# Kernel optimization log

Hardware: AMD Instinct MI355X
Metric: run time of the kernel (lower is better)

Reference implementation:

```python
import jax, jax.numpy as jnp
import numpy as np

B, T, C = 8, 1024, 768
H = 12
HS = C // H  # 64


def setup_inputs() -> dict:
    key = jax.random.key(0)
    ks = jax.random.split(key, 6)
    s = C ** -0.5
    x = jax.random.normal(ks[0], (B, T, C), dtype=jnp.float32)
    Wq = jax.random.normal(ks[1], (H, C, HS), dtype=jnp.float32) * s
    Wk = jax.random.normal(ks[2], (H, C, HS), dtype=jnp.float32) * s
    Wv = jax.random.normal(ks[3], (H, C, HS), dtype=jnp.float32) * s
    Wproj = jax.random.normal(ks[4], (C, C), dtype=jnp.float32) * s
    bproj = jax.random.normal(ks[5], (C,), dtype=jnp.float32) * 0.01
    return {"x": x, "Wq": Wq, "Wk": Wk, "Wv": Wv, "Wproj": Wproj, "bproj": bproj}


def reference(x, Wq, Wk, Wv, Wproj, bproj):
    # per-head projections (equivalent to stacked per-head nn.Linear, bias=False)
    q = jnp.einsum('btc,hcd->bhtd', x, Wq)
    k = jnp.einsum('btc,hcd->bhtd', x, Wk)
    v = jnp.einsum('btc,hcd->bhtd', x, Wv)
    scale = HS ** -0.5
    scores = jnp.einsum('bhtd,bhsd->bhts', q, k) * scale  # [B,H,T,T]
    causal = jnp.tril(jnp.ones((T, T), dtype=bool))
    scores = jnp.where(causal, scores, -jnp.inf)
    weights = jax.nn.softmax(scores, axis=-1)
    out = jnp.einsum('bhts,bhsd->bhtd', weights, v)  # [B,H,T,HS]
    out = out.transpose(0, 2, 1, 3).reshape(B, T, C)  # concat heads
    # output projection (dropout is identity in eval mode)
    return out @ Wproj.T + bproj
```

## Files before the change

kernel.cpp:

```cpp
#include <hip/hip_runtime.h>


typedef short bf16x8 __attribute__((ext_vector_type(8)));
typedef float f32x4 __attribute__((ext_vector_type(4)));

static __device__ __forceinline__ unsigned short f2bf(float f) {
  unsigned int u = __float_as_uint(f);
  u += 0x7fffu + ((u >> 16) & 1u);
  return (unsigned short)(u >> 16);
}

static __device__ __forceinline__ void gl_lds16(const void* g, void* l) {
  __builtin_amdgcn_global_load_lds(
      (const __attribute__((address_space(1))) unsigned int*)g,
      (__attribute__((address_space(3))) unsigned int*)l, 16, 0, 0);
}

__global__ __launch_bounds__(256) void k_prep(
    const float* __restrict__ x, const float* __restrict__ Wproj,
    const float* __restrict__ Wq, const float* __restrict__ Wk,
    const float* __restrict__ Wv,
    unsigned short* __restrict__ xb, unsigned short* __restrict__ wp,
    unsigned short* __restrict__ wt) {
  __shared__ float tb[64][65];
  const int bx = blockIdx.x;
  const int tid = threadIdx.x;
  if (bx < 6720) {
    const float* src = (bx < 6144) ? x : Wproj;
    unsigned short* dst = (bx < 6144) ? xb : wp;
    int i = (bx < 6144 ? bx : bx - 6144) * 256 + tid;
    float4 f = ((const float4*)src)[i];
    ushort4 o;
    o.x = f2bf(f.x); o.y = f2bf(f.y); o.z = f2bf(f.z); o.w = f2bf(f.w);
    ((ushort4*)dst)[i] = o;
    return;
  }
  const int idx = bx - 6720;
  const int c0 = (idx % 12) * 64;
  const int hq = idx / 12;
  const int qi = hq / 12, h = hq % 12;
  const float* W = (qi == 0) ? Wq : ((qi == 1) ? Wk : Wv);
  {
    int rowb = tid >> 4;
    int col4 = (tid & 15) * 4;
#pragma unroll
    for (int it = 0; it < 4; ++it) {
      int c = it * 16 + rowb;
      float4 f = *(const float4*)(W + (h * 768 + c0 + c) * 64 + col4);
      tb[c][col4] = f.x; tb[c][col4 + 1] = f.y; tb[c][col4 + 2] = f.z; tb[c][col4 + 3] = f.w;
    }
  }
  __syncthreads();
#pragma unroll
  for (int it = 0; it < 2; ++it) {
    int slot = it * 256 + tid;
    int d = slot >> 3, cg = (slot & 7) * 8;
    union { unsigned short a[8]; uint4 v; } o;
#pragma unroll
    for (int j = 0; j < 8; ++j) o.a[j] = f2bf(tb[cg + j][d]);
    *(uint4*)(wt + (qi * 768 + h * 64 + d) * 768 + c0 + cg) = o.v;
  }
}

__global__ __launch_bounds__(256) void k_gemm_qk(
    const unsigned short* __restrict__ xb,
    const unsigned short* __restrict__ wt,
    unsigned short* __restrict__ qkv) {
  __shared__ unsigned short As[128 * 32];
  __shared__ unsigned short Bs[128 * 32];
  const int tid = threadIdx.x;
  const int w = tid >> 6, lane = tid & 63, quad = lane >> 4, lr = lane & 15;
  const int wm = w >> 1, wn = w & 1;
  const int m0 = blockIdx.x * 128, n0 = blockIdx.y * 128;

  f32x4 acc[4][4] = {};

  const int srow = w * 16 + (lane >> 2);
  const int scol = (lane & 3) * 8;
  const unsigned short* ga0 = xb + (m0 + srow) * 768 + scol;
  const unsigned short* ga1 = ga0 + 64 * 768;
  const unsigned short* gb0 = wt + (n0 + srow) * 768 + scol;
  const unsigned short* gb1 = gb0 + 64 * 768;
  unsigned short* la0 = &As[(w * 16) * 32];
  unsigned short* la1 = la0 + 64 * 32;
  unsigned short* lb0 = &Bs[(w * 16) * 32];
  unsigned short* lb1 = lb0 + 64 * 32;

  for (int k0 = 0; k0 < 768; k0 += 32) {
    gl_lds16(ga0 + k0, la0);
    gl_lds16(ga1 + k0, la1);
    gl_lds16(gb0 + k0, lb0);
    gl_lds16(gb1 + k0, lb1);
    __syncthreads();
    bf16x8 af[4], bfr[4];
#pragma unroll
    for (int i = 0; i < 4; ++i)
      af[i] = *(const bf16x8*)(&As[(wm * 64 + i * 16 + lr) * 32 + quad * 8]);
#pragma unroll
    for (int j = 0; j < 4; ++j)
      bfr[j] = *(const bf16x8*)(&Bs[(wn * 64 + j * 16 + lr) * 32 + quad * 8]);
#pragma unroll
    for (int i = 0; i < 4; ++i)
#pragma unroll
      for (int j = 0; j < 4; ++j)
        acc[i][j] = __builtin_amdgcn_mfma_f32_16x16x32_bf16(af[i], bfr[j], acc[i][j], 0, 0, 0);
    __syncthreads();
  }

  const int b = m0 >> 10, t0 = m0 & 1023;
#pragma unroll
  for (int j = 0; j < 4; ++j) {
    int n = n0 + wn * 64 + j * 16 + lr;
    int qi = n >> 9 >> 1;
    qi = n / 768;
    int rr = n - qi * 768;
    int h = rr >> 6, d = rr & 63;
#pragma unroll
    for (int i = 0; i < 4; ++i) {
#pragma unroll
      for (int r = 0; r < 4; ++r) {
        int t = t0 + wm * 64 + i * 16 + quad * 4 + r;
        qkv[(size_t)(((qi * 8 + b) * 12 + h) * 1024 + t) * 64 + d] = f2bf(acc[i][j][r]);
      }
    }
  }
}

__global__ __launch_bounds__(256) void k_gemm_v(
    const unsigned short* __restrict__ xb,
    const unsigned short* __restrict__ wt,
    unsigned short* __restrict__ vt) {
  __shared__ unsigned short As[128 * 32];
  __shared__ unsigned short Bs[128 * 32];
  const int tid = threadIdx.x;
  const int w = tid >> 6, lane = tid & 63, quad = lane >> 4, lr = lane & 15;
  const int wm = w >> 1, wn = w & 1;
  const int m0 = blockIdx.x * 128, n0 = blockIdx.y * 128;

  f32x4 acc[4][4] = {};

  const int srow = w * 16 + (lane >> 2);
  const int scol = (lane & 3) * 8;
  const unsigned short* ga0 = xb + (m0 + srow) * 768 + scol;
  const unsigned short* ga1 = ga0 + 64 * 768;
  const unsigned short* gb0 = wt + (size_t)(1536 + n0 + srow) * 768 + scol;
  const unsigned short* gb1 = gb0 + 64 * 768;
  unsigned short* la0 = &As[(w * 16) * 32];
  unsigned short* la1 = la0 + 64 * 32;
  unsigned short* lb0 = &Bs[(w * 16) * 32];
  unsigned short* lb1 = lb0 + 64 * 32;

  for (int k0 = 0; k0 < 768; k0 += 32) {
    gl_lds16(ga0 + k0, la0);
    gl_lds16(ga1 + k0, la1);
    gl_lds16(gb0 + k0, lb0);
    gl_lds16(gb1 + k0, lb1);
    __syncthreads();
    bf16x8 af[4], bfr[4];
#pragma unroll
    for (int i = 0; i < 4; ++i)
      af[i] = *(const bf16x8*)(&As[(wm * 64 + i * 16 + lr) * 32 + quad * 8]);
#pragma unroll
    for (int j = 0; j < 4; ++j)
      bfr[j] = *(const bf16x8*)(&Bs[(wn * 64 + j * 16 + lr) * 32 + quad * 8]);
#pragma unroll
    for (int i = 0; i < 4; ++i)
#pragma unroll
      for (int j = 0; j < 4; ++j)
        acc[i][j] = __builtin_amdgcn_mfma_f32_16x16x32_bf16(af[i], bfr[j], acc[i][j], 0, 0, 0);
    __syncthreads();
  }

  const int b = m0 >> 10, t0 = m0 & 1023;
#pragma unroll
  for (int j = 0; j < 4; ++j) {
    int rr = n0 + wn * 64 + j * 16 + lr;
    int h = rr >> 6, d = rr & 63;
    unsigned short* vrow = vt + (size_t)((b * 12 + h) * 64 + d) * 1024;
#pragma unroll
    for (int i = 0; i < 4; ++i) {
      int t = t0 + wm * 64 + i * 16 + quad * 4;
      union { unsigned short a[4]; uint2 u; } o;
#pragma unroll
      for (int r = 0; r < 4; ++r) o.a[r] = f2bf(acc[i][j][r]);
      *(uint2*)(vrow + t) = o.u;
    }
  }
}

__global__ __launch_bounds__(256) void k_attn(
    const unsigned short* __restrict__ qkv,
    const unsigned short* __restrict__ Vtg,
    unsigned short* __restrict__ attn) {
  __shared__ unsigned short Kbuf[2][64 * 64];
  __shared__ unsigned short Vbuf[2][64 * 64];
  __shared__ unsigned short Pbuf[4][32 * 68];
  const int tid = threadIdx.x;
  const int w = tid >> 6, lane = tid & 63, quad = lane >> 4, lr = lane & 15;
  const int hb = blockIdx.x;
  const int qb = 7 - (int)blockIdx.y;
  const int h = hb % 12, b = hb / 12;
  const int HT = 65536;
  const unsigned short* Q  = qkv + (b * 12 + h) * HT;
  const unsigned short* K  = qkv + (96 + b * 12 + h) * HT;
  const unsigned short* Vt = Vtg + (b * 12 + h) * HT;

  bf16x8 aq[2][2];
#pragma unroll
  for (int i = 0; i < 2; ++i)
#pragma unroll
    for (int hf = 0; hf < 2; ++hf)
      aq[i][hf] = *(const bf16x8*)(Q + (qb * 128 + w * 32 + i * 16 + lr) * 64 + hf * 32 + quad * 8);

  f32x4 accO[2][4] = {};
  float lsum[2][4] = {};

  const int nc = 2 * qb + 2;
  const float c1 = 0.125f * 1.4426950408889634f;
  const float c0 = -4.0f * 1.4426950408889634f;

  auto stage = [&](int bi, int sc) {
#pragma unroll
    for (int j = 0; j < 2; ++j) {
      int row = w * 16 + j * 8 + (lane >> 3);
      int c8 = (lane & 7) ^ (row & 7);
      gl_lds16(K + (sc * 64 + row) * 64 + c8 * 8, &Kbuf[bi][(w * 16 + j * 8) * 64]);
      gl_lds16(Vt + row * 1024 + sc * 64 + c8 * 8, &Vbuf[bi][(w * 16 + j * 8) * 64]);
    }
  };

  stage(0, 0);
  for (int sc = 0; sc < nc; ++sc) {
    __syncthreads();
    if (sc + 1 < nc) stage((sc + 1) & 1, sc + 1);
    const unsigned short* Kl = Kbuf[sc & 1];
    const unsigned short* Vl = Vbuf[sc & 1];

    f32x4 accS[2][4];
#pragma unroll
    for (int i = 0; i < 2; ++i)
#pragma unroll
      for (int nt = 0; nt < 4; ++nt) {
        f32x4 z = {};
#pragma unroll
        for (int hf = 0; hf < 2; ++hf) {
          int s = nt * 16 + lr;
          bf16x8 kb = *(const bf16x8*)(Kl + (s * 8 + ((4 * hf + quad) ^ (s & 7))) * 8);
          z = __builtin_amdgcn_mfma_f32_16x16x32_bf16(aq[i][hf], kb, z, 0, 0, 0);
        }
        accS[i][nt] = z;
      }

#pragma unroll
    for (int i = 0; i < 2; ++i) {
      const int base_i = qb * 128 + w * 32 + i * 16;
      const bool needmask = (sc * 64 + 63 > base_i);
#pragma unroll
      for (int r = 0; r < 4; ++r) {
        int tg = base_i + quad * 4 + r;
#pragma unroll
        for (int nt = 0; nt < 4; ++nt) {
          float p = __builtin_amdgcn_exp2f(fmaf(accS[i][nt][r], c1, c0));
          if (needmask && (sc * 64 + nt * 16 + lr > tg)) p = 0.f;
          lsum[i][r] += p;
          Pbuf[w][(i * 16 + quad * 4 + r) * 68 + nt * 16 + lr] = f2bf(p);
        }
      }
    }

#pragma unroll
    for (int i = 0; i < 2; ++i) {
      bf16x8 pa[2];
#pragma unroll
      for (int hf = 0; hf < 2; ++hf)
        pa[hf] = *(const bf16x8*)(&Pbuf[w][(i * 16 + lr) * 68 + hf * 32 + quad * 8]);
#pragma unroll
      for (int ntd = 0; ntd < 4; ++ntd) {
        int d = ntd * 16 + lr;
#pragma unroll
        for (int hf = 0; hf < 2; ++hf) {
          bf16x8 vb = *(const bf16x8*)(Vl + (d * 8 + ((4 * hf + quad) ^ (d & 7))) * 8);
          accO[i][ntd] = __builtin_amdgcn_mfma_f32_16x16x32_bf16(pa[hf], vb, accO[i][ntd], 0, 0, 0);
        }
      }
    }
  }

  float linv[2][4];
#pragma unroll
  for (int i = 0; i < 2; ++i)
#pragma unroll
    for (int r = 0; r < 4; ++r) {
      float l = lsum[i][r];
      l += __shfl_xor(l, 1);
      l += __shfl_xor(l, 2);
      l += __shfl_xor(l, 4);
      l += __shfl_xor(l, 8);
      linv[i][r] = 1.0f / l;
    }

#pragma unroll
  for (int i = 0; i < 2; ++i)
#pragma unroll
    for (int ntd = 0; ntd < 4; ++ntd) {
      int c = h * 64 + ntd * 16 + lr;
#pragma unroll
      for (int r = 0; r < 4; ++r) {
        int t = qb * 128 + w * 32 + i * 16 + quad * 4 + r;
        attn[(b * 1024 + t) * 768 + c] = f2bf(accO[i][ntd][r] * linv[i][r]);
      }
    }
}

__global__ __launch_bounds__(256) void k_gemm_proj(
    const unsigned short* __restrict__ ab,
    const unsigned short* __restrict__ wp,
    const float* __restrict__ bias,
    float* __restrict__ out) {
  __shared__ unsigned short As[128 * 32];
  __shared__ unsigned short Bs[128 * 32];
  const int tid = threadIdx.x;
  const int w = tid >> 6, lane = tid & 63, quad = lane >> 4, lr = lane & 15;
  const int wm = w >> 1, wn = w & 1;
  const int m0 = blockIdx.x * 128, n0 = blockIdx.y * 128;

  f32x4 acc[4][4] = {};

  const int srow = w * 16 + (lane >> 2);
  const int scol = (lane & 3) * 8;
  const unsigned short* ga0 = ab + (m0 + srow) * 768 + scol;
  const unsigned short* ga1 = ga0 + 64 * 768;
  const unsigned short* gb0 = wp + (n0 + srow) * 768 + scol;
  const unsigned short* gb1 = gb0 + 64 * 768;
  unsigned short* la0 = &As[(w * 16) * 32];
  unsigned short* la1 = la0 + 64 * 32;
  unsigned short* lb0 = &Bs[(w * 16) * 32];
  unsigned short* lb1 = lb0 + 64 * 32;

  for (int k0 = 0; k0 < 768; k0 += 32) {
    gl_lds16(ga0 + k0, la0);
    gl_lds16(ga1 + k0, la1);
    gl_lds16(gb0 + k0, lb0);
    gl_lds16(gb1 + k0, lb1);
    __syncthreads();
    bf16x8 af[4], bfr[4];
#pragma unroll
    for (int i = 0; i < 4; ++i)
      af[i] = *(const bf16x8*)(&As[(wm * 64 + i * 16 + lr) * 32 + quad * 8]);
#pragma unroll
    for (int j = 0; j < 4; ++j)
      bfr[j] = *(const bf16x8*)(&Bs[(wn * 64 + j * 16 + lr) * 32 + quad * 8]);
#pragma unroll
    for (int i = 0; i < 4; ++i)
#pragma unroll
      for (int j = 0; j < 4; ++j)
        acc[i][j] = __builtin_amdgcn_mfma_f32_16x16x32_bf16(af[i], bfr[j], acc[i][j], 0, 0, 0);
    __syncthreads();
  }

#pragma unroll
  for (int j = 0; j < 4; ++j) {
    int ncol = n0 + wn * 64 + j * 16 + lr;
    float bv = bias[ncol];
#pragma unroll
    for (int i = 0; i < 4; ++i) {
#pragma unroll
      for (int r = 0; r < 4; ++r) {
        int m = m0 + wm * 64 + i * 16 + quad * 4 + r;
        out[(size_t)m * 768 + ncol] = acc[i][j][r] + bv;
      }
    }
  }
}

extern "C" void kernel_launch(void* const* d_in, const int* in_sizes, int n_in,
                              void* d_out, int out_size, void* d_ws, size_t ws_size,
                              hipStream_t stream) {
  const float* x     = (const float*)d_in[0];
  const float* Wq    = (const float*)d_in[1];
  const float* Wk    = (const float*)d_in[2];
  const float* Wv    = (const float*)d_in[3];
  const float* Wproj = (const float*)d_in[4];
  const float* bproj = (const float*)d_in[5];
  float* out = (float*)d_out;

  char* p = (char*)d_ws;
  unsigned short* xb   = (unsigned short*)p; p += 12582912;
  unsigned short* wt   = (unsigned short*)p; p += 3538944;
  unsigned short* wp   = (unsigned short*)p; p += 1179648;
  unsigned short* qkv  = (unsigned short*)p; p += 37748736;
  unsigned short* attn = (unsigned short*)p; p += 12582912;
  unsigned short* vt   = qkv + (size_t)192 * 65536;

  k_prep<<<7152, 256, 0, stream>>>(x, Wproj, Wq, Wk, Wv, xb, wp, wt);
  k_gemm_qk<<<dim3(64, 12), 256, 0, stream>>>(xb, wt, qkv);
  k_gemm_v<<<dim3(64, 6), 256, 0, stream>>>(xb, wt, vt);
  k_attn<<<dim3(96, 8), 256, 0, stream>>>(qkv, vt, attn);
  k_gemm_proj<<<dim3(64, 6), 256, 0, stream>>>(attn, wp, bproj, out);
}
```

Measured before the change: 192.8 us.

## Transpose MFMA operands to vectorize epilogue stores and keep attention P in registers

The QKV and projection GEMMs swap the MFMA A/B operands, so each lane holds four consecutive output columns and can write packed bf16 or float4 stores instead of scalar ones. The attention kernel computes S transposed (K times Q), so the softmax probabilities land in the register layout the 16x16x16 MFMA expects as its B operand. This removes the Pbuf LDS round trip, simplifies the row-sum reduction, and vectorizes the output stores. It also adds a launch-bounds occupancy hint. The trade-off is twice as many smaller MFMAs for P·V and 8-byte LDS reads of V.

```diff
diff --git a/kernel.cpp b/kernel.cpp
--- a/kernel.cpp
+++ b/kernel.cpp
@@ -2,12 +2,21 @@
 
 
 typedef short bf16x8 __attribute__((ext_vector_type(8)));
+typedef short bf16x4 __attribute__((ext_vector_type(4)));
 typedef float f32x4 __attribute__((ext_vector_type(4)));
 
 static __device__ __forceinline__ unsigned short f2bf(float f) {
   unsigned int u = __float_as_uint(f);
   u += 0x7fffu + ((u >> 16) & 1u);
   return (unsigned short)(u >> 16);
+}
+
+static __device__ __forceinline__ unsigned int pk2bf(float a, float b) {
+  unsigned int ua = __float_as_uint(a);
+  ua += 0x7fffu + ((ua >> 16) & 1u);
+  unsigned int ub = __float_as_uint(b);
+  ub += 0x7fffu + ((ub >> 16) & 1u);
+  return (ua >> 16) | (ub & 0xffff0000u);
 }
 
 static __device__ __forceinline__ void gl_lds16(const void* g, void* l) {
@@ -100,28 +109,28 @@
     for (int j = 0; j < 4; ++j)
       bfr[j] = *(const bf16x8*)(&Bs[(wn * 64 + j * 16 + lr) * 32 + quad * 8]);
 #pragma unroll
-    for (int i = 0; i < 4; ++i)
-#pragma unroll
-      for (int j = 0; j < 4; ++j)
-        acc[i][j] = __builtin_amdgcn_mfma_f32_16x16x32_bf16(af[i], bfr[j], acc[i][j], 0, 0, 0);
+    for (int j = 0; j < 4; ++j)
+#pragma unroll
+      for (int i = 0; i < 4; ++i)
+        acc[j][i] = __builtin_amdgcn_mfma_f32_16x16x32_bf16(bfr[j], af[i], acc[j][i], 0, 0, 0);
     __syncthreads();
   }
 
   const int b = m0 >> 10, t0 = m0 & 1023;
+  const int qi = n0 / 768;
+  const int rr0 = n0 - qi * 768;
 #pragma unroll
   for (int j = 0; j < 4; ++j) {
-    int n = n0 + wn * 64 + j * 16 + lr;
-    int qi = n >> 9 >> 1;
-    qi = n / 768;
-    int rr = n - qi * 768;
-    int h = rr >> 6, d = rr & 63;
+    int nn = rr0 + wn * 64 + j * 16 + quad * 4;
+    int h = nn >> 6, d0 = nn & 63;
+    unsigned short* hb = qkv + (size_t)((qi * 8 + b) * 12 + h) * 65536 + d0;
 #pragma unroll
     for (int i = 0; i < 4; ++i) {
-#pragma unroll
-      for (int r = 0; r < 4; ++r) {
-        int t = t0 + wm * 64 + i * 16 + quad * 4 + r;
-        qkv[(size_t)(((qi * 8 + b) * 12 + h) * 1024 + t) * 64 + d] = f2bf(acc[i][j][r]);
-      }
+      int t = t0 + wm * 64 + i * 16 + lr;
+      union { unsigned int u[2]; uint2 v; } o;
+      o.u[0] = pk2bf(acc[j][i][0], acc[j][i][1]);
+      o.u[1] = pk2bf(acc[j][i][2], acc[j][i][3]);
+      *(uint2*)(hb + (size_t)t * 64) = o.v;
     }
   }
 }
@@ -180,21 +189,20 @@
 #pragma unroll
     for (int i = 0; i < 4; ++i) {
       int t = t0 + wm * 64 + i * 16 + quad * 4;
-      union { unsigned short a[4]; uint2 u; } o;
-#pragma unroll
-      for (int r = 0; r < 4; ++r) o.a[r] = f2bf(acc[i][j][r]);
-      *(uint2*)(vrow + t) = o.u;
-    }
-  }
-}
-
-__global__ __launch_bounds__(256) void k_attn(
+      union { unsigned int u[2]; uint2 v; } o;
+      o.u[0] = pk2bf(acc[i][j][0], acc[i][j][1]);
+      o.u[1] = pk2bf(acc[i][j][2], acc[i][j][3]);
+      *(uint2*)(vrow + t) = o.v;
+    }
+  }
+}
+
+__global__ __launch_bounds__(256, 4) void k_attn(
     const unsigned short* __restrict__ qkv,
     const unsigned short* __restrict__ Vtg,
     unsigned short* __restrict__ attn) {
   __shared__ unsigned short Kbuf[2][64 * 64];
   __shared__ unsigned short Vbuf[2][64 * 64];
-  __shared__ unsigned short Pbuf[4][32 * 68];
   const int tid = threadIdx.x;
   const int w = tid >> 6, lane = tid & 63, quad = lane >> 4, lr = lane & 15;
   const int hb = blockIdx.x;
@@ -205,15 +213,15 @@
   const unsigned short* K  = qkv + (96 + b * 12 + h) * HT;
   const unsigned short* Vt = Vtg + (b * 12 + h) * HT;
 
-  bf16x8 aq[2][2];
+  bf16x8 bq[2][2];
 #pragma unroll
   for (int i = 0; i < 2; ++i)
 #pragma unroll
     for (int hf = 0; hf < 2; ++hf)
-      aq[i][hf] = *(const bf16x8*)(Q + (qb * 128 + w * 32 + i * 16 + lr) * 64 + hf * 32 + quad * 8);
+      bq[i][hf] = *(const bf16x8*)(Q + (qb * 128 + w * 32 + i * 16 + lr) * 64 + hf * 32 + quad * 8);
 
   f32x4 accO[2][4] = {};
-  float lsum[2][4] = {};
+  float lsum[2] = {};
 
   const int nc = 2 * qb + 2;
   const float c1 = 0.125f * 1.4426950408889634f;
@@ -236,7 +244,7 @@
     const unsigned short* Kl = Kbuf[sc & 1];
     const unsigned short* Vl = Vbuf[sc & 1];
 
-    f32x4 accS[2][4];
+    f32x4 accT[2][4];
 #pragma unroll
     for (int i = 0; i < 2; ++i)
 #pragma unroll
@@ -246,70 +254,70 @@
         for (int hf = 0; hf < 2; ++hf) {
           int s = nt * 16 + lr;
           bf16x8 kb = *(const bf16x8*)(Kl + (s * 8 + ((4 * hf + quad) ^ (s & 7))) * 8);
-          z = __builtin_amdgcn_mfma_f32_16x16x32_bf16(aq[i][hf], kb, z, 0, 0, 0);
+          z = __builtin_amdgcn_mfma_f32_16x16x32_bf16(kb, bq[i][hf], z, 0, 0, 0);
         }
-        accS[i][nt] = z;
+        accT[i][nt] = z;
       }
 
+    bf16x4 pb[2][4];
 #pragma unroll
     for (int i = 0; i < 2; ++i) {
       const int base_i = qb * 128 + w * 32 + i * 16;
       const bool needmask = (sc * 64 + 63 > base_i);
-#pragma unroll
-      for (int r = 0; r < 4; ++r) {
-        int tg = base_i + quad * 4 + r;
-#pragma unroll
-        for (int nt = 0; nt < 4; ++nt) {
-          float p = __builtin_amdgcn_exp2f(fmaf(accS[i][nt][r], c1, c0));
-          if (needmask && (sc * 64 + nt * 16 + lr > tg)) p = 0.f;
-          lsum[i][r] += p;
-          Pbuf[w][(i * 16 + quad * 4 + r) * 68 + nt * 16 + lr] = f2bf(p);
+      const int q_l = base_i + lr;
+#pragma unroll
+      for (int st = 0; st < 4; ++st) {
+        float p[4];
+#pragma unroll
+        for (int r = 0; r < 4; ++r) {
+          float e = __builtin_amdgcn_exp2f(fmaf(accT[i][st][r], c1, c0));
+          if (needmask && (sc * 64 + st * 16 + quad * 4 + r > q_l)) e = 0.f;
+          lsum[i] += e;
+          p[r] = e;
         }
+        union { unsigned int u[2]; bf16x4 v; } pk;
+        pk.u[0] = pk2bf(p[0], p[1]);
+        pk.u[1] = pk2bf(p[2], p[3]);
+        pb[i][st] = pk.v;
       }
     }
 
 #pragma unroll
-    for (int i = 0; i < 2; ++i) {
-      bf16x8 pa[2];
-#pragma unroll
-      for (int hf = 0; hf < 2; ++hf)
-        pa[hf] = *(const bf16x8*)(&Pbuf[w][(i * 16 + lr) * 68 + hf * 32 + quad * 8]);
-#pragma unroll
-      for (int ntd = 0; ntd < 4; ++ntd) {
+    for (int ntd = 0; ntd < 4; ++ntd) {
+#pragma unroll
+      for (int st = 0; st < 4; ++st) {
         int d = ntd * 16 + lr;
-#pragma unroll
-        for (int hf = 0; hf < 2; ++hf) {
-          bf16x8 vb = *(const bf16x8*)(Vl + (d * 8 + ((4 * hf + quad) ^ (d & 7))) * 8);
-          accO[i][ntd] = __builtin_amdgcn_mfma_f32_16x16x32_bf16(pa[hf], vb, accO[i][ntd], 0, 0, 0);
-        }
+        int u = st * 2 + (quad >> 1);
+        int us = u ^ (d & 7);
+        bf16x4 va = *(const bf16x4*)(Vl + d * 64 + us * 8 + (quad & 1) * 4);
+#pragma unroll
+        for (int i = 0; i < 2; ++i)
+          accO[i][ntd] = __builtin_amdgcn_mfma_f32_16x16x16bf16_1k(va, pb[i][st], accO[i][ntd], 0, 0, 0);
       }
     }
   }
 
-  float linv[2][4];
-#pragma unroll
-  for (int i = 0; i < 2; ++i)
-#pragma unroll
-    for (int r = 0; r < 4; ++r) {
-      float l = lsum[i][r];
-      l += __shfl_xor(l, 1);
-      l += __shfl_xor(l, 2);
-      l += __shfl_xor(l, 4);
-      l += __shfl_xor(l, 8);
-      linv[i][r] = 1.0f / l;
-    }
-
-#pragma unroll
-  for (int i = 0; i < 2; ++i)
+  float linv[2];
+#pragma unroll
+  for (int i = 0; i < 2; ++i) {
+    float l = lsum[i];
+    l += __shfl_xor(l, 16);
+    l += __shfl_xor(l, 32);
+    linv[i] = 1.0f / l;
+  }
+
+#pragma unroll
+  for (int i = 0; i < 2; ++i) {
+    int t = qb * 128 + w * 32 + i * 16 + lr;
+    unsigned short* row = attn + (size_t)(b * 1024 + t) * 768 + h * 64 + quad * 4;
 #pragma unroll
     for (int ntd = 0; ntd < 4; ++ntd) {
-      int c = h * 64 + ntd * 16 + lr;
-#pragma unroll
-      for (int r = 0; r < 4; ++r) {
-        int t = qb * 128 + w * 32 + i * 16 + quad * 4 + r;
-        attn[(b * 1024 + t) * 768 + c] = f2bf(accO[i][ntd][r] * linv[i][r]);
-      }
-    }
+      union { unsigned int u[2]; uint2 v; } o;
+      o.u[0] = pk2bf(accO[i][ntd][0] * linv[i], accO[i][ntd][1] * linv[i]);
+      o.u[1] = pk2bf(accO[i][ntd][2] * linv[i], accO[i][ntd][3] * linv[i]);
+      *(uint2*)(row + ntd * 16) = o.v;
+    }
+  }
 }
 
 __global__ __launch_bounds__(256) void k_gemm_proj(
@@ -351,24 +359,26 @@
     for (int j = 0; j < 4; ++j)
       bfr[j] = *(const bf16x8*)(&Bs[(wn * 64 + j * 16 + lr) * 32 + quad * 8]);
 #pragma unroll
-    for (int i = 0; i < 4; ++i)
-#pragma unroll
-      for (int j = 0; j < 4; ++j)
-        acc[i][j] = __builtin_amdgcn_mfma_f32_16x16x32_bf16(af[i], bfr[j], acc[i][j], 0, 0, 0);
+    for (int j = 0; j < 4; ++j)
+#pragma unroll
+      for (int i = 0; i < 4; ++i)
+        acc[j][i] = __builtin_amdgcn_mfma_f32_16x16x32_bf16(bfr[j], af[i], acc[j][i], 0, 0, 0);
     __syncthreads();
   }
 
 #pragma unroll
   for (int j = 0; j < 4; ++j) {
-    int ncol = n0 + wn * 64 + j * 16 + lr;
-    float bv = bias[ncol];
+    int ncol = n0 + wn * 64 + j * 16 + quad * 4;
+    float4 bv = *(const float4*)(bias + ncol);
 #pragma unroll
     for (int i = 0; i < 4; ++i) {
-#pragma unroll
-      for (int r = 0; r < 4; ++r) {
-        int m = m0 + wm * 64 + i * 16 + quad * 4 + r;
-        out[(size_t)m * 768 + ncol] = acc[i][j][r] + bv;
-      }
+      int m = m0 + wm * 64 + i * 16 + lr;
+      float4 v;
+      v.x = acc[j][i][0] + bv.x;
+      v.y = acc[j][i][1] + bv.y;
+      v.z = acc[j][i][2] + bv.z;
+      v.w = acc[j][i][3] + bv.w;
+      *(float4*)(out + (size_t)m * 768 + ncol) = v;
     }
   }
 }
```

Result: no change. 193.4 us (+0.3%).
